# Kernel optimization log

Measured on AMD Instinct MI355X. Metric: run time of the kernel, lower is better.

## Reference

```python
import jax, jax.numpy as jnp
import numpy as np
from jax import lax

THETA = 0.7
DN = ('NCHW', 'OIHW', 'NCHW')


def setup_inputs() -> dict:
    key = jax.random.key(0)
    k1, k2 = jax.random.split(key)
    x = jax.random.normal(k1, (16, 64, 128, 128), dtype=jnp.float32)
    W = jax.random.normal(k2, (64, 64, 3, 3), dtype=jnp.float32) * 0.05
    return {"x": x, "W": W}


def _shift_sum(x):
    # Sum of the center view plus the 8 shifted views of the reflection-padded
    # input (the original code's lt/mt/rt/lm/center/mr/ld/md/rd slices cover
    # exactly the full 3x3 neighborhood of the padded tensor).
    B, C, H, W_ = x.shape
    xp = jnp.pad(x, ((0, 0), (0, 0), (1, 1), (1, 1)), mode='reflect')
    s = jnp.zeros_like(x)
    for dy in range(3):
        for dx in range(3):
            s = s + xp[:, :, dy:dy + H, dx:dx + W_]
    return s


def reference(x, W):
    # Conv is linear and bias=False, so sum_i conv(shift_i(x)) == conv(sum_i shift_i(x)).
    s = _shift_sum(x)  # [B,C,H,W]
    out_normal = lax.conv_general_dilated(s, W, (1, 1), [(1, 1), (1, 1)], dimension_numbers=DN)
    kernel_diff = W.sum(axis=(2, 3))[:, :, None, None]  # [C_out,C_in,1,1]
    out_diff = lax.conv_general_dilated(s, kernel_diff, (1, 1), [(0, 0), (0, 0)], dimension_numbers=DN)
    return out_normal - THETA * out_diff
```

## Files before the change

### kernel.cpp

```cpp
#include <hip/hip_runtime.h>
#include <stdint.h>


#define THETA 0.7f

typedef __attribute__((ext_vector_type(8))) short bf16x8;
typedef __attribute__((ext_vector_type(16))) float f32x16;

__device__ inline unsigned short f2bf(float f) {
    unsigned u = __float_as_uint(f);
    u = (u + 0x7FFFu + ((u >> 16) & 1u)) >> 16;
    return (unsigned short)u;
}
__device__ inline void async16(const void* g, void* l) {
    __builtin_amdgcn_global_load_lds(
        (const __attribute__((address_space(1))) unsigned int*)g,
        (__attribute__((address_space(3))) unsigned int*)l, 16, 0, 0);
}

__global__ void weff_kernel(const float* __restrict__ W, unsigned short* __restrict__ Wt2) {
    int t = blockIdx.x * blockDim.x + threadIdx.x;
    if (t >= 512) return;
    int o = t >> 3;
    int ch8 = t & 7;
    int c0 = ch8 * 8;
    int ic = ch8 >> 1;
    int mf = o >> 5;
    int lane = (o & 31) | ((ch8 & 1) << 5);

    float v[8][9];
    float tsum[8];
#pragma unroll
    for (int j = 0; j < 8; j++) {
        const float* w = W + ((size_t)o * 64 + c0 + j) * 9;
        float sum = 0.f;
#pragma unroll
        for (int k = 0; k < 9; k++) { v[j][k] = w[k]; sum += v[j][k]; }
        tsum[j] = sum;
    }
#pragma unroll
    for (int tap = 0; tap < 9; tap++) {
        unsigned short* dst = Wt2 + (((size_t)(tap * 4 + ic) * 2 + mf) * 64 + lane) * 8;
#pragma unroll
        for (int j = 0; j < 8; j++) {
            float val = v[j][tap] - ((tap == 4) ? THETA * tsum[j] : 0.f);
            dst[j] = f2bf(val);
        }
    }
}

__global__ __launch_bounds__(512) void boxsumT_kernel(const float* __restrict__ x,
                                                      unsigned short* __restrict__ s) {
    __shared__ unsigned short tb[128 * 72];
    int bid = blockIdx.x;
    int b = bid >> 4;
    int h0 = (bid & 15) * 8;
    int tid = threadIdx.x;
    int w4 = tid & 31;
    int cg = tid >> 5;
    int c0 = cg * 4;
    const float* xp = x + ((size_t)(b * 64 + c0)) * 16384 + w4 * 4;

    float4 A[4], B[4], C[4];
    int hm = (h0 == 0) ? 1 : h0 - 1;
#pragma unroll
    for (int cc = 0; cc < 4; cc++) {
        A[cc] = *(const float4*)(xp + (size_t)cc * 16384 + hm * 128);
        B[cc] = *(const float4*)(xp + (size_t)cc * 16384 + h0 * 128);
        C[cc] = *(const float4*)(xp + (size_t)cc * 16384 + (h0 + 1) * 128);
    }

#pragma unroll
    for (int r = 0; r < 8; r++) {
        float4 Cn[4];
        if (r < 7) {
            int hn = h0 + 2 + r;
            if (hn > 127) hn = 126;
#pragma unroll
            for (int cc = 0; cc < 4; cc++)
                Cn[cc] = *(const float4*)(xp + (size_t)cc * 16384 + hn * 128);
        }

        unsigned short res[4][4];
#pragma unroll
        for (int cc = 0; cc < 4; cc++) {
            float4 vs;
            vs.x = A[cc].x + B[cc].x + C[cc].x;
            vs.y = A[cc].y + B[cc].y + C[cc].y;
            vs.z = A[cc].z + B[cc].z + C[cc].z;
            vs.w = A[cc].w + B[cc].w + C[cc].w;
            float L = __shfl_up(vs.w, 1, 32);
            float R = __shfl_down(vs.x, 1, 32);
            float sx = (w4 == 0) ? vs.x + 2.f * vs.y : L + vs.x + vs.y;
            float sy = vs.x + vs.y + vs.z;
            float sz = vs.y + vs.z + vs.w;
            float sw = (w4 == 31) ? 2.f * vs.z + vs.w : vs.z + vs.w + R;
            res[cc][0] = f2bf(sx);
            res[cc][1] = f2bf(sy);
            res[cc][2] = f2bf(sz);
            res[cc][3] = f2bf(sw);
        }
#pragma unroll
        for (int k = 0; k < 4; k++) {
            ushort4 o4 = make_ushort4(res[0][k], res[1][k], res[2][k], res[3][k]);
            *(ushort4*)(tb + (size_t)(w4 * 4 + k) * 72 + c0) = o4;
        }
#pragma unroll
        for (int cc = 0; cc < 4; cc++) { A[cc] = B[cc]; B[cc] = C[cc]; C[cc] = Cn[cc]; }
        __syncthreads();

        unsigned short* sp = s + (((size_t)b * 128 + (h0 + r)) * 128) * 64;
#pragma unroll
        for (int f = 0; f < 2; f++) {
            int id = f * 512 + tid;
            int w = id >> 3, c8 = id & 7;
            bf16x8 v = *(const bf16x8*)(tb + (size_t)w * 72 + c8 * 8);
            *(bf16x8*)(sp + (size_t)w * 64 + c8 * 8) = v;
        }
        __syncthreads();
    }
}

__global__ __launch_bounds__(256, 2) void conv_kernel(const unsigned short* __restrict__ s,
                                                      const unsigned short* __restrict__ Wt2,
                                                      float* __restrict__ out) {
    __shared__ __align__(16) unsigned short sS[6 * 66 * 64];

    int bid = blockIdx.x;
    int b = bid >> 6;
    int h0 = ((bid >> 1) & 31) * 4;
    int w0 = (bid & 1) * 64;
    int tid = threadIdx.x;
    int lane = tid & 63;
    int wv = tid >> 6;
    int n32 = lane & 31;
    int q2 = lane >> 5;

    const char* sb = (const char*)s + ((size_t)b * 128) * 16384;

    int4 z = make_int4(0, 0, 0, 0);
    if (h0 == 0)
        for (int i = tid; i < 528; i += 256) *(int4*)((char*)sS + (size_t)i * 16) = z;
    if (h0 == 124)
        for (int i = tid; i < 528; i += 256) *(int4*)((char*)sS + (size_t)(5 * 528 + i) * 16) = z;

    if (tid < 96) {
        int r = tid >> 4;
        int side = (tid >> 3) & 1;
        int g = tid & 7;
        int slot = side ? 65 : 0;
        int hg = h0 - 1 + r;
        int wg = w0 - 1 + slot;
        int4 v = z;
        if ((unsigned)hg < 128u && (unsigned)wg < 128u) {
            int u = g ^ (slot & 7);
            v = *(const int4*)(sb + (size_t)hg * 16384 + (size_t)wg * 128 + u * 16);
        }
        *(int4*)((char*)sS + (size_t)(r * 528 + slot * 8 + g) * 16) = v;
    }

#pragma unroll
    for (int it = 0; it < 12; it++) {
        int row = it >> 1;
        int hg = h0 - 1 + row;
        if (hg < 0 || hg > 127) continue;
        int rem = (it & 1) * 256 + tid;
        int slot = 1 + (rem >> 3);
        int g = rem & 7;
        int wg = w0 + (rem >> 3);
        int u = g ^ (slot & 7);
        async16(sb + (size_t)hg * 16384 + (size_t)wg * 128 + u * 16,
                (char*)sS + (size_t)(row * 528 + 8 + rem) * 16);
    }
    __syncthreads();

    int p0[3][4];
#pragma unroll
    for (int kx = 0; kx < 3; kx++)
#pragma unroll
        for (int ic = 0; ic < 4; ic++) {
            int slot = n32 + kx;
            int g = (ic * 2 + q2) ^ (slot & 7);
            p0[kx][ic] = slot * 64 + g * 8;
        }

    f32x16 acc[2][2];
#pragma unroll
    for (int mf = 0; mf < 2; mf++)
#pragma unroll
        for (int nf = 0; nf < 2; nf++)
#pragma unroll
            for (int r = 0; r < 16; r++) acc[mf][nf][r] = 0.f;

    bf16x8 Af[8], An[8];
#pragma unroll
    for (int ic = 0; ic < 4; ic++)
#pragma unroll
        for (int mf = 0; mf < 2; mf++)
            Af[ic * 2 + mf] = *(const bf16x8*)(Wt2 + (((size_t)(0 * 4 + ic) * 2 + mf) * 64 + lane) * 8);

#pragma unroll
    for (int tap = 0; tap < 9; tap++) {
        int ky = tap / 3, kx = tap % 3;
        if (tap < 8) {
#pragma unroll
            for (int ic = 0; ic < 4; ic++)
#pragma unroll
                for (int mf = 0; mf < 2; mf++)
                    An[ic * 2 + mf] = *(const bf16x8*)(Wt2 + (((size_t)((tap + 1) * 4 + ic) * 2 + mf) * 64 + lane) * 8);
        }
#pragma unroll
        for (int ic = 0; ic < 4; ic++) {
            const unsigned short* bp = sS + (size_t)(wv + ky) * 4224 + p0[kx][ic];
            bf16x8 b0 = *(const bf16x8*)(bp);
            bf16x8 b1 = *(const bf16x8*)(bp + 2048);
            acc[0][0] = __builtin_amdgcn_mfma_f32_32x32x16_bf16(Af[ic * 2 + 0], b0, acc[0][0], 0, 0, 0);
            acc[0][1] = __builtin_amdgcn_mfma_f32_32x32x16_bf16(Af[ic * 2 + 0], b1, acc[0][1], 0, 0, 0);
            acc[1][0] = __builtin_amdgcn_mfma_f32_32x32x16_bf16(Af[ic * 2 + 1], b0, acc[1][0], 0, 0, 0);
            acc[1][1] = __builtin_amdgcn_mfma_f32_32x32x16_bf16(Af[ic * 2 + 1], b1, acc[1][1], 0, 0, 0);
        }
        if (tap < 8) {
#pragma unroll
            for (int k = 0; k < 8; k++) Af[k] = An[k];
        }
    }

    float* ob = out + ((size_t)b * 64) * 16384 + (size_t)(h0 + wv) * 128 + w0;
#pragma unroll
    for (int mf = 0; mf < 2; mf++)
#pragma unroll
        for (int nf = 0; nf < 2; nf++)
#pragma unroll
            for (int r = 0; r < 16; r++) {
                int o = mf * 32 + (r & 3) + 8 * (r >> 2) + 4 * q2;
                ob[(size_t)o * 16384 + nf * 32 + n32] = acc[mf][nf][r];
            }
}

extern "C" void kernel_launch(void* const* d_in, const int* in_sizes, int n_in,
                              void* d_out, int out_size, void* d_ws, size_t ws_size,
                              hipStream_t stream) {
    const float* x = (const float*)d_in[0];
    const float* W = (const float*)d_in[1];
    float* outp = (float*)d_out;

    unsigned short* Wt2 = (unsigned short*)d_ws;
    unsigned short* s = (unsigned short*)((char*)d_ws + 73728);

    weff_kernel<<<2, 256, 0, stream>>>(W, Wt2);
    boxsumT_kernel<<<256, 512, 0, stream>>>(x, s);
    conv_kernel<<<1024, 256, 0, stream>>>(s, Wt2, outp);
}
```

Baseline: 142.1 us.

## Fuse box-sum computation into conv kernel, dropping intermediate bf16 buffer

```diff
diff --git a/kernel.cpp b/kernel.cpp
--- a/kernel.cpp
+++ b/kernel.cpp
@@ -11,11 +11,6 @@
     unsigned u = __float_as_uint(f);
     u = (u + 0x7FFFu + ((u >> 16) & 1u)) >> 16;
     return (unsigned short)u;
-}
-__device__ inline void async16(const void* g, void* l) {
-    __builtin_amdgcn_global_load_lds(
-        (const __attribute__((address_space(1))) unsigned int*)g,
-        (__attribute__((address_space(3))) unsigned int*)l, 16, 0, 0);
 }
 
 __global__ void weff_kernel(const float* __restrict__ W, unsigned short* __restrict__ Wt2) {
@@ -49,81 +44,49 @@
     }
 }
 
-__global__ __launch_bounds__(512) void boxsumT_kernel(const float* __restrict__ x,
-                                                      unsigned short* __restrict__ s) {
-    __shared__ unsigned short tb[128 * 72];
-    int bid = blockIdx.x;
-    int b = bid >> 4;
-    int h0 = (bid & 15) * 8;
-    int tid = threadIdx.x;
-    int w4 = tid & 31;
-    int cg = tid >> 5;
-    int c0 = cg * 4;
-    const float* xp = x + ((size_t)(b * 64 + c0)) * 16384 + w4 * 4;
+template<bool LEDGE>
+__device__ __forceinline__ void stage_row(const float* __restrict__ xb,
+                                          unsigned short* sSp,
+                                          int h0, int row, int c) {
+    int hg = h0 - 1 + row;
+    if (hg < 0 || hg > 127) return;
+    const float* r0 = xb + (size_t)((hg == 0) ? 1 : hg - 1) * 128;
+    const float* r1 = xb + (size_t)hg * 128;
+    const float* r2 = xb + (size_t)((hg == 127) ? 126 : hg + 1) * 128;
+    constexpr int xw0 = LEDGE ? 0 : 60;
+    constexpr int joff = LEDGE ? 2 : -2;
 
-    float4 A[4], B[4], C[4];
-    int hm = (h0 == 0) ? 1 : h0 - 1;
+    float v[68];
 #pragma unroll
-    for (int cc = 0; cc < 4; cc++) {
-        A[cc] = *(const float4*)(xp + (size_t)cc * 16384 + hm * 128);
-        B[cc] = *(const float4*)(xp + (size_t)cc * 16384 + h0 * 128);
-        C[cc] = *(const float4*)(xp + (size_t)cc * 16384 + (h0 + 1) * 128);
+    for (int k = 0; k < 17; k++) {
+        float4 a = *(const float4*)(r0 + xw0 + 4 * k);
+        float4 bb = *(const float4*)(r1 + xw0 + 4 * k);
+        float4 cc = *(const float4*)(r2 + xw0 + 4 * k);
+        float s4[4] = {a.x + bb.x + cc.x, a.y + bb.y + cc.y,
+                       a.z + bb.z + cc.z, a.w + bb.w + cc.w};
+#pragma unroll
+        for (int e = 0; e < 4; e++) {
+            int j = 4 * k + e + joff;
+            if (j >= 0 && j < 68) v[j] = s4[e];
+        }
     }
+    if (LEDGE) { v[0] = v[4]; v[1] = v[3]; }
+    else       { v[66] = v[64]; v[67] = v[63]; }
 
+    unsigned short* base = sSp + row * 4224 + (c & 7);
+    int u8 = c >> 3;
 #pragma unroll
-    for (int r = 0; r < 8; r++) {
-        float4 Cn[4];
-        if (r < 7) {
-            int hn = h0 + 2 + r;
-            if (hn > 127) hn = 126;
-#pragma unroll
-            for (int cc = 0; cc < 4; cc++)
-                Cn[cc] = *(const float4*)(xp + (size_t)cc * 16384 + hn * 128);
-        }
-
-        unsigned short res[4][4];
-#pragma unroll
-        for (int cc = 0; cc < 4; cc++) {
-            float4 vs;
-            vs.x = A[cc].x + B[cc].x + C[cc].x;
-            vs.y = A[cc].y + B[cc].y + C[cc].y;
-            vs.z = A[cc].z + B[cc].z + C[cc].z;
-            vs.w = A[cc].w + B[cc].w + C[cc].w;
-            float L = __shfl_up(vs.w, 1, 32);
-            float R = __shfl_down(vs.x, 1, 32);
-            float sx = (w4 == 0) ? vs.x + 2.f * vs.y : L + vs.x + vs.y;
-            float sy = vs.x + vs.y + vs.z;
-            float sz = vs.y + vs.z + vs.w;
-            float sw = (w4 == 31) ? 2.f * vs.z + vs.w : vs.z + vs.w + R;
-            res[cc][0] = f2bf(sx);
-            res[cc][1] = f2bf(sy);
-            res[cc][2] = f2bf(sz);
-            res[cc][3] = f2bf(sw);
-        }
-#pragma unroll
-        for (int k = 0; k < 4; k++) {
-            ushort4 o4 = make_ushort4(res[0][k], res[1][k], res[2][k], res[3][k]);
-            *(ushort4*)(tb + (size_t)(w4 * 4 + k) * 72 + c0) = o4;
-        }
-#pragma unroll
-        for (int cc = 0; cc < 4; cc++) { A[cc] = B[cc]; B[cc] = C[cc]; C[cc] = Cn[cc]; }
-        __syncthreads();
-
-        unsigned short* sp = s + (((size_t)b * 128 + (h0 + r)) * 128) * 64;
-#pragma unroll
-        for (int f = 0; f < 2; f++) {
-            int id = f * 512 + tid;
-            int w = id >> 3, c8 = id & 7;
-            bf16x8 v = *(const bf16x8*)(tb + (size_t)w * 72 + c8 * 8);
-            *(bf16x8*)(sp + (size_t)w * 64 + c8 * 8) = v;
-        }
-        __syncthreads();
+    for (int slot = 0; slot < 66; slot++) {
+        float sv = v[slot] + v[slot + 1] + v[slot + 2];
+        if (LEDGE && slot == 0) sv = 0.f;
+        if (!LEDGE && slot == 65) sv = 0.f;
+        base[slot * 64 + ((u8 ^ (slot & 7)) << 3)] = f2bf(sv);
     }
 }
 
-__global__ __launch_bounds__(256, 2) void conv_kernel(const unsigned short* __restrict__ s,
-                                                      const unsigned short* __restrict__ Wt2,
-                                                      float* __restrict__ out) {
+__global__ __launch_bounds__(256, 2) void fused_kernel(const float* __restrict__ x,
+                                                       const unsigned short* __restrict__ Wt2,
+                                                       float* __restrict__ out) {
     __shared__ __align__(16) unsigned short sS[6 * 66 * 64];
 
     int bid = blockIdx.x;
@@ -136,41 +99,30 @@
     int n32 = lane & 31;
     int q2 = lane >> 5;
 
-    const char* sb = (const char*)s + ((size_t)b * 128) * 16384;
-
     int4 z = make_int4(0, 0, 0, 0);
     if (h0 == 0)
         for (int i = tid; i < 528; i += 256) *(int4*)((char*)sS + (size_t)i * 16) = z;
     if (h0 == 124)
         for (int i = tid; i < 528; i += 256) *(int4*)((char*)sS + (size_t)(5 * 528 + i) * 16) = z;
 
-    if (tid < 96) {
-        int r = tid >> 4;
-        int side = (tid >> 3) & 1;
-        int g = tid & 7;
-        int slot = side ? 65 : 0;
-        int hg = h0 - 1 + r;
-        int wg = w0 - 1 + slot;
-        int4 v = z;
-        if ((unsigned)hg < 128u && (unsigned)wg < 128u) {
-            int u = g ^ (slot & 7);
-            v = *(const int4*)(sb + (size_t)hg * 16384 + (size_t)wg * 128 + u * 16);
+    bf16x8 Af[8], An[8];
+#pragma unroll
+    for (int ic = 0; ic < 4; ic++)
+#pragma unroll
+        for (int mf = 0; mf < 2; mf++)
+            Af[ic * 2 + mf] = *(const bf16x8*)(Wt2 + (((size_t)(0 * 4 + ic) * 2 + mf) * 64 + lane) * 8);
+
+    {
+        int c = lane;
+        int rw = wv;
+        const float* xb = x + ((size_t)(b * 64 + c)) * 16384;
+        if (w0 == 0) {
+            stage_row<true>(xb, sS, h0, rw, c);
+            if (rw < 2) stage_row<true>(xb, sS, h0, 4 + rw, c);
+        } else {
+            stage_row<false>(xb, sS, h0, rw, c);
+            if (rw < 2) stage_row<false>(xb, sS, h0, 4 + rw, c);
         }
-        *(int4*)((char*)sS + (size_t)(r * 528 + slot * 8 + g) * 16) = v;
-    }
-
-#pragma unroll
-    for (int it = 0; it < 12; it++) {
-        int row = it >> 1;
-        int hg = h0 - 1 + row;
-        if (hg < 0 || hg > 127) continue;
-        int rem = (it & 1) * 256 + tid;
-        int slot = 1 + (rem >> 3);
-        int g = rem & 7;
-        int wg = w0 + (rem >> 3);
-        int u = g ^ (slot & 7);
-        async16(sb + (size_t)hg * 16384 + (size_t)wg * 128 + u * 16,
-                (char*)sS + (size_t)(row * 528 + 8 + rem) * 16);
     }
     __syncthreads();
 
@@ -191,13 +143,6 @@
         for (int nf = 0; nf < 2; nf++)
 #pragma unroll
             for (int r = 0; r < 16; r++) acc[mf][nf][r] = 0.f;
-
-    bf16x8 Af[8], An[8];
-#pragma unroll
-    for (int ic = 0; ic < 4; ic++)
-#pragma unroll
-        for (int mf = 0; mf < 2; mf++)
-            Af[ic * 2 + mf] = *(const bf16x8*)(Wt2 + (((size_t)(0 * 4 + ic) * 2 + mf) * 64 + lane) * 8);
 
 #pragma unroll
     for (int tap = 0; tap < 9; tap++) {
@@ -245,9 +190,7 @@
     float* outp = (float*)d_out;
 
     unsigned short* Wt2 = (unsigned short*)d_ws;
-    unsigned short* s = (unsigned short*)((char*)d_ws + 73728);
 
     weff_kernel<<<2, 256, 0, stream>>>(W, Wt2);
-    boxsumT_kernel<<<256, 512, 0, stream>>>(x, s);
-    conv_kernel<<<1024, 256, 0, stream>>>(s, Wt2, outp);
+    fused_kernel<<<1024, 256, 0, stream>>>(x, Wt2, outp);
 }
```

Result: slower. 168.8 us (+18.8%).

## Fuse box-sum into conv kernel, computing halo rows in shared memory

Applied to the files above, without the earlier changes.

```diff
diff --git a/kernel.cpp b/kernel.cpp
--- a/kernel.cpp
+++ b/kernel.cpp
@@ -11,11 +11,6 @@
     unsigned u = __float_as_uint(f);
     u = (u + 0x7FFFu + ((u >> 16) & 1u)) >> 16;
     return (unsigned short)u;
-}
-__device__ inline void async16(const void* g, void* l) {
-    __builtin_amdgcn_global_load_lds(
-        (const __attribute__((address_space(1))) unsigned int*)g,
-        (__attribute__((address_space(3))) unsigned int*)l, 16, 0, 0);
 }
 
 __global__ void weff_kernel(const float* __restrict__ W, unsigned short* __restrict__ Wt2) {
@@ -49,128 +44,103 @@
     }
 }
 
-__global__ __launch_bounds__(512) void boxsumT_kernel(const float* __restrict__ x,
-                                                      unsigned short* __restrict__ s) {
-    __shared__ unsigned short tb[128 * 72];
+__global__ __launch_bounds__(512, 2) void fused_kernel(const float* __restrict__ x,
+                                                       const unsigned short* __restrict__ Wt2,
+                                                       float* __restrict__ out) {
+    __shared__ __align__(16) unsigned short sS[6 * 132 * 64];
+
     int bid = blockIdx.x;
-    int b = bid >> 4;
-    int h0 = (bid & 15) * 8;
-    int tid = threadIdx.x;
-    int w4 = tid & 31;
-    int cg = tid >> 5;
-    int c0 = cg * 4;
-    const float* xp = x + ((size_t)(b * 64 + c0)) * 16384 + w4 * 4;
-
-    float4 A[4], B[4], C[4];
-    int hm = (h0 == 0) ? 1 : h0 - 1;
-#pragma unroll
-    for (int cc = 0; cc < 4; cc++) {
-        A[cc] = *(const float4*)(xp + (size_t)cc * 16384 + hm * 128);
-        B[cc] = *(const float4*)(xp + (size_t)cc * 16384 + h0 * 128);
-        C[cc] = *(const float4*)(xp + (size_t)cc * 16384 + (h0 + 1) * 128);
-    }
-
-#pragma unroll
-    for (int r = 0; r < 8; r++) {
-        float4 Cn[4];
-        if (r < 7) {
-            int hn = h0 + 2 + r;
-            if (hn > 127) hn = 126;
-#pragma unroll
-            for (int cc = 0; cc < 4; cc++)
-                Cn[cc] = *(const float4*)(xp + (size_t)cc * 16384 + hn * 128);
-        }
-
-        unsigned short res[4][4];
-#pragma unroll
-        for (int cc = 0; cc < 4; cc++) {
-            float4 vs;
-            vs.x = A[cc].x + B[cc].x + C[cc].x;
-            vs.y = A[cc].y + B[cc].y + C[cc].y;
-            vs.z = A[cc].z + B[cc].z + C[cc].z;
-            vs.w = A[cc].w + B[cc].w + C[cc].w;
-            float L = __shfl_up(vs.w, 1, 32);
-            float R = __shfl_down(vs.x, 1, 32);
-            float sx = (w4 == 0) ? vs.x + 2.f * vs.y : L + vs.x + vs.y;
-            float sy = vs.x + vs.y + vs.z;
-            float sz = vs.y + vs.z + vs.w;
-            float sw = (w4 == 31) ? 2.f * vs.z + vs.w : vs.z + vs.w + R;
-            res[cc][0] = f2bf(sx);
-            res[cc][1] = f2bf(sy);
-            res[cc][2] = f2bf(sz);
-            res[cc][3] = f2bf(sw);
-        }
-#pragma unroll
-        for (int k = 0; k < 4; k++) {
-            ushort4 o4 = make_ushort4(res[0][k], res[1][k], res[2][k], res[3][k]);
-            *(ushort4*)(tb + (size_t)(w4 * 4 + k) * 72 + c0) = o4;
-        }
-#pragma unroll
-        for (int cc = 0; cc < 4; cc++) { A[cc] = B[cc]; B[cc] = C[cc]; C[cc] = Cn[cc]; }
-        __syncthreads();
-
-        unsigned short* sp = s + (((size_t)b * 128 + (h0 + r)) * 128) * 64;
-#pragma unroll
-        for (int f = 0; f < 2; f++) {
-            int id = f * 512 + tid;
-            int w = id >> 3, c8 = id & 7;
-            bf16x8 v = *(const bf16x8*)(tb + (size_t)w * 72 + c8 * 8);
-            *(bf16x8*)(sp + (size_t)w * 64 + c8 * 8) = v;
-        }
-        __syncthreads();
-    }
-}
-
-__global__ __launch_bounds__(256, 2) void conv_kernel(const unsigned short* __restrict__ s,
-                                                      const unsigned short* __restrict__ Wt2,
-                                                      float* __restrict__ out) {
-    __shared__ __align__(16) unsigned short sS[6 * 66 * 64];
-
-    int bid = blockIdx.x;
-    int b = bid >> 6;
-    int h0 = ((bid >> 1) & 31) * 4;
-    int w0 = (bid & 1) * 64;
+    int b = bid >> 5;
+    int h0 = (bid & 31) * 4;
     int tid = threadIdx.x;
     int lane = tid & 63;
     int wv = tid >> 6;
     int n32 = lane & 31;
     int q2 = lane >> 5;
-
-    const char* sb = (const char*)s + ((size_t)b * 128) * 16384;
+    int orow = wv >> 1;
+    int whalf = wv & 1;
 
     int4 z = make_int4(0, 0, 0, 0);
+    if (tid < 96) {
+        int rr = tid >> 4;
+        int sl = ((tid & 15) >> 3) ? 129 : 0;
+        int g = tid & 7;
+        *(int4*)((char*)sS + ((size_t)(rr * 132 + sl) * 8 + g) * 16) = z;
+    }
     if (h0 == 0)
-        for (int i = tid; i < 528; i += 256) *(int4*)((char*)sS + (size_t)i * 16) = z;
+        for (int i = tid; i < 1056; i += 512) *(int4*)((char*)sS + (size_t)i * 16) = z;
     if (h0 == 124)
-        for (int i = tid; i < 528; i += 256) *(int4*)((char*)sS + (size_t)(5 * 528 + i) * 16) = z;
-
-    if (tid < 96) {
-        int r = tid >> 4;
-        int side = (tid >> 3) & 1;
-        int g = tid & 7;
-        int slot = side ? 65 : 0;
-        int hg = h0 - 1 + r;
-        int wg = w0 - 1 + slot;
-        int4 v = z;
-        if ((unsigned)hg < 128u && (unsigned)wg < 128u) {
-            int u = g ^ (slot & 7);
-            v = *(const int4*)(sb + (size_t)hg * 16384 + (size_t)wg * 128 + u * 16);
-        }
-        *(int4*)((char*)sS + (size_t)(r * 528 + slot * 8 + g) * 16) = v;
-    }
-
-#pragma unroll
-    for (int it = 0; it < 12; it++) {
-        int row = it >> 1;
-        int hg = h0 - 1 + row;
-        if (hg < 0 || hg > 127) continue;
-        int rem = (it & 1) * 256 + tid;
-        int slot = 1 + (rem >> 3);
-        int g = rem & 7;
-        int wg = w0 + (rem >> 3);
-        int u = g ^ (slot & 7);
-        async16(sb + (size_t)hg * 16384 + (size_t)wg * 128 + u * 16,
-                (char*)sS + (size_t)(row * 528 + 8 + rem) * 16);
+        for (int i = tid; i < 1056; i += 512) *(int4*)((char*)sS + (size_t)(5280 + i) * 16) = z;
+
+    bf16x8 Af[8], An[8];
+#pragma unroll
+    for (int ic = 0; ic < 4; ic++)
+#pragma unroll
+        for (int mf = 0; mf < 2; mf++)
+            Af[ic * 2 + mf] = *(const bf16x8*)(Wt2 + (((size_t)(0 * 4 + ic) * 2 + mf) * 64 + lane) * 8);
+
+    {
+        int w4 = tid & 31;
+        int cg = tid >> 5;
+        int c0 = cg * 4;
+        int u8 = cg >> 1;
+        int hh = (cg & 1) * 4;
+        const float* xp = x + ((size_t)(b * 64 + c0)) * 16384 + w4 * 4;
+
+        int hgf = (h0 == 0) ? 0 : h0 - 1;
+        int hm = (hgf == 0) ? 1 : hgf - 1;
+        float4 A[4], Bv[4], C[4];
+#pragma unroll
+        for (int cc = 0; cc < 4; cc++) {
+            A[cc]  = *(const float4*)(xp + (size_t)cc * 16384 + (size_t)hm * 128);
+            Bv[cc] = *(const float4*)(xp + (size_t)cc * 16384 + (size_t)hgf * 128);
+            C[cc]  = *(const float4*)(xp + (size_t)cc * 16384 + (size_t)(hgf + 1) * 128);
+        }
+
+#pragma unroll
+        for (int rr = 0; rr < 6; rr++) {
+            int hg = h0 - 1 + rr;
+            if (hg < 0 || hg > 127) continue;
+
+            float4 Cn[4];
+            if (rr < 5) {
+                int hn = hg + 2;
+                if (hn > 127) hn = 126;
+#pragma unroll
+                for (int cc = 0; cc < 4; cc++)
+                    Cn[cc] = *(const float4*)(xp + (size_t)cc * 16384 + (size_t)hn * 128);
+            }
+
+            unsigned short res[4][4];
+#pragma unroll
+            for (int cc = 0; cc < 4; cc++) {
+                float4 vs;
+                vs.x = A[cc].x + Bv[cc].x + C[cc].x;
+                vs.y = A[cc].y + Bv[cc].y + C[cc].y;
+                vs.z = A[cc].z + Bv[cc].z + C[cc].z;
+                vs.w = A[cc].w + Bv[cc].w + C[cc].w;
+                float L = __shfl_up(vs.w, 1, 32);
+                float R = __shfl_down(vs.x, 1, 32);
+                float sx = (w4 == 0) ? vs.x + 2.f * vs.y : L + vs.x + vs.y;
+                float sy = vs.x + vs.y + vs.z;
+                float sz = vs.y + vs.z + vs.w;
+                float sw_ = (w4 == 31) ? 2.f * vs.z + vs.w : vs.z + vs.w + R;
+                res[cc][0] = f2bf(sx);
+                res[cc][1] = f2bf(sy);
+                res[cc][2] = f2bf(sz);
+                res[cc][3] = f2bf(sw_);
+            }
+#pragma unroll
+            for (int k = 0; k < 4; k++) {
+                int slot = w4 * 4 + k + 1;
+                ushort4 o4 = make_ushort4(res[0][k], res[1][k], res[2][k], res[3][k]);
+                *(ushort4*)(sS + (size_t)(rr * 132 + slot) * 64 + ((u8 ^ (slot & 7)) << 3) + hh) = o4;
+            }
+            if (rr < 5) {
+#pragma unroll
+                for (int cc = 0; cc < 4; cc++) { A[cc] = Bv[cc]; Bv[cc] = C[cc]; C[cc] = Cn[cc]; }
+            }
+        }
     }
     __syncthreads();
 
@@ -179,7 +149,7 @@
     for (int kx = 0; kx < 3; kx++)
 #pragma unroll
         for (int ic = 0; ic < 4; ic++) {
-            int slot = n32 + kx;
+            int slot = n32 + kx + whalf * 64;
             int g = (ic * 2 + q2) ^ (slot & 7);
             p0[kx][ic] = slot * 64 + g * 8;
         }
@@ -191,13 +161,6 @@
         for (int nf = 0; nf < 2; nf++)
 #pragma unroll
             for (int r = 0; r < 16; r++) acc[mf][nf][r] = 0.f;
-
-    bf16x8 Af[8], An[8];
-#pragma unroll
-    for (int ic = 0; ic < 4; ic++)
-#pragma unroll
-        for (int mf = 0; mf < 2; mf++)
-            Af[ic * 2 + mf] = *(const bf16x8*)(Wt2 + (((size_t)(0 * 4 + ic) * 2 + mf) * 64 + lane) * 8);
 
 #pragma unroll
     for (int tap = 0; tap < 9; tap++) {
@@ -211,7 +174,7 @@
         }
 #pragma unroll
         for (int ic = 0; ic < 4; ic++) {
-            const unsigned short* bp = sS + (size_t)(wv + ky) * 4224 + p0[kx][ic];
+            const unsigned short* bp = sS + (size_t)(orow + ky) * 8448 + p0[kx][ic];
             bf16x8 b0 = *(const bf16x8*)(bp);
             bf16x8 b1 = *(const bf16x8*)(bp + 2048);
             acc[0][0] = __builtin_amdgcn_mfma_f32_32x32x16_bf16(Af[ic * 2 + 0], b0, acc[0][0], 0, 0, 0);
@@ -225,7 +188,7 @@
         }
     }
 
-    float* ob = out + ((size_t)b * 64) * 16384 + (size_t)(h0 + wv) * 128 + w0;
+    float* ob = out + ((size_t)b * 64) * 16384 + (size_t)(h0 + orow) * 128 + whalf * 64;
 #pragma unroll
     for (int mf = 0; mf < 2; mf++)
 #pragma unroll
@@ -245,9 +208,7 @@
     float* outp = (float*)d_out;
 
     unsigned short* Wt2 = (unsigned short*)d_ws;
-    unsigned short* s = (unsigned short*)((char*)d_ws + 73728);
 
     weff_kernel<<<2, 256, 0, stream>>>(W, Wt2);
-    boxsumT_kernel<<<256, 512, 0, stream>>>(x, s);
-    conv_kernel<<<1024, 256, 0, stream>>>(s, Wt2, outp);
-}
+    fused_kernel<<<512, 512, 0, stream>>>(x, Wt2, outp);
+}
```

After: 142.9 us. Within noise of the previous version (+0.6%).
